# Kernel tuning notes

Measured on AMD Instinct MI355X. Metric: run time of the kernel, lower is better.

## Reference

```python
import jax, jax.numpy as jnp
import numpy as np

HIDDEN = 2048
VOCAB = 50257


def setup_inputs() -> dict:
    key = jax.random.key(0)
    ks = jax.random.split(key, 9)
    s = 0.02
    return {
        "token": jax.random.randint(ks[0], (1,), 0, VOCAB, dtype=jnp.int32),
        "hidden": jax.random.normal(ks[1], (1, 1, HIDDEN), dtype=jnp.float32),
        "emb": jax.random.normal(ks[2], (VOCAB, HIDDEN), dtype=jnp.float32) * s,
        "w_ih": jax.random.normal(ks[3], (3 * HIDDEN, HIDDEN), dtype=jnp.float32) * s,
        "w_hh": jax.random.normal(ks[4], (3 * HIDDEN, HIDDEN), dtype=jnp.float32) * s,
        "b_ih": jax.random.normal(ks[5], (3 * HIDDEN,), dtype=jnp.float32) * s,
        "b_hh": jax.random.normal(ks[6], (3 * HIDDEN,), dtype=jnp.float32) * s,
        "w_out": jax.random.normal(ks[7], (VOCAB, HIDDEN), dtype=jnp.float32) * s,
        "b_out": jax.random.normal(ks[8], (VOCAB,), dtype=jnp.float32) * s,
    }


def reference(token, hidden, emb, w_ih, w_hh, b_ih, b_hh, w_out, b_out):
    # embedding lookup + view(1,1,-1) + ReLU  -> x: [H]
    x = jax.nn.relu(emb[token].reshape(-1))
    h = hidden.reshape(-1)  # [H]
    # single GRU step (PyTorch gate order: r, z, n; separate input/hidden biases)
    gi = w_ih @ x + b_ih  # [3H]
    gh = w_hh @ h + b_hh  # [3H]
    i_r, i_z, i_n = jnp.split(gi, 3)
    h_r, h_z, h_n = jnp.split(gh, 3)
    r = jax.nn.sigmoid(i_r + h_r)
    z = jax.nn.sigmoid(i_z + h_z)
    n = jnp.tanh(i_n + r * h_n)
    h_new = (1.0 - z) * n + z * h  # [H]
    # output projection + log-softmax over vocab (dim=1 of [1, V])
    logits = w_out @ h_new + b_out  # [V]
    out = jax.nn.log_softmax(logits)[None, :]  # [1, V]
    return out, h_new.reshape(1, 1, -1)
```

## Files before the change

kernel.cpp:

```cpp
#include <hip/hip_runtime.h>
#include <math.h>

#define H 2048
#define G 6144
#define V 50257

#define WS_GI    0
#define WS_GH    G
#define WS_HNEW  12288
#define WS_MAX   14336
#define WS_SUM   14337
#define WS_LOGIT 14344

__device__ __forceinline__ float waveReduceSum(float v) {
  #pragma unroll
  for (int off = 32; off > 0; off >>= 1) v += __shfl_down(v, off, 64);
  return v;
}
__device__ __forceinline__ float waveReduceMax(float v) {
  #pragma unroll
  for (int off = 32; off > 0; off >>= 1) v = fmaxf(v, __shfl_down(v, off, 64));
  return v;
}

__device__ __forceinline__ unsigned orderedBits(float f) {
  unsigned u = __float_as_uint(f);
  return (u & 0x80000000u) ? ~u : (u | 0x80000000u);
}
__device__ __forceinline__ float orderedToFloat(unsigned m) {
  unsigned u = (m & 0x80000000u) ? (m & 0x7fffffffu) : ~m;
  return __uint_as_float(u);
}

__global__ __launch_bounds__(256) void gates_kernel(
    const int* __restrict__ token, const float* __restrict__ hidden,
    const float* __restrict__ emb, const float* __restrict__ w_ih,
    const float* __restrict__ w_hh, const float* __restrict__ b_ih,
    const float* __restrict__ b_hh, float* __restrict__ ws) {
  const int wave = threadIdx.x >> 6;
  const int lane = threadIdx.x & 63;
  const int row = blockIdx.x * 4 + wave;
  if (row >= G) return;
  const float4* x4 = (const float4*)(emb + (size_t)token[0] * H);
  const float4* h4 = (const float4*)hidden;
  const float4* wi = (const float4*)(w_ih + (size_t)row * H);
  const float4* wh = (const float4*)(w_hh + (size_t)row * H);
  float si = 0.f, sh = 0.f;
  #pragma unroll
  for (int k = 0; k < 8; ++k) {
    const int idx = k * 64 + lane;
    float4 a = wi[idx];
    float4 b = x4[idx];
    si += a.x * fmaxf(b.x, 0.f) + a.y * fmaxf(b.y, 0.f)
        + a.z * fmaxf(b.z, 0.f) + a.w * fmaxf(b.w, 0.f);
    float4 c = wh[idx];
    float4 d = h4[idx];
    sh += c.x * d.x + c.y * d.y + c.z * d.z + c.w * d.w;
  }
  si = waveReduceSum(si);
  sh = waveReduceSum(sh);
  if (lane == 0) {
    ws[WS_GI + row] = si + b_ih[row];
    ws[WS_GH + row] = sh + b_hh[row];
  }
}

__global__ __launch_bounds__(256) void hnew_kernel(
    const float* __restrict__ hidden, float* __restrict__ ws,
    float* __restrict__ out) {
  const int i = blockIdx.x * blockDim.x + threadIdx.x;
  if (i == 0) {
    ((unsigned*)ws)[WS_MAX] = 0u;
    ws[WS_SUM] = 0.f;
  }
  if (i < H) {
    const float r = 1.f / (1.f + expf(-(ws[WS_GI + i] + ws[WS_GH + i])));
    const float z = 1.f / (1.f + expf(-(ws[WS_GI + H + i] + ws[WS_GH + H + i])));
    const float n = tanhf(ws[WS_GI + 2 * H + i] + r * ws[WS_GH + 2 * H + i]);
    const float hn = (1.f - z) * n + z * hidden[i];
    ws[WS_HNEW + i] = hn;
    out[V + i] = hn;
  }
}

__global__ __launch_bounds__(256) void logits_kernel(
    const float* __restrict__ w_out, const float* __restrict__ b_out,
    float* __restrict__ ws) {
  const int wave = threadIdx.x >> 6;
  const int lane = threadIdx.x & 63;
  const int row = blockIdx.x * 4 + wave;
  if (row >= V) return;
  const float4* w4 = (const float4*)(w_out + (size_t)row * H);
  const float4* h4 = (const float4*)(ws + WS_HNEW);
  float s = 0.f;
  #pragma unroll
  for (int k = 0; k < 8; ++k) {
    const int idx = k * 64 + lane;
    float4 a = w4[idx];
    float4 b = h4[idx];
    s += a.x * b.x + a.y * b.y + a.z * b.z + a.w * b.w;
  }
  s = waveReduceSum(s);
  if (lane == 0) ws[WS_LOGIT + row] = s + b_out[row];
}

__global__ __launch_bounds__(256) void max_kernel(float* __restrict__ ws) {
  float m = -INFINITY;
  for (int i = blockIdx.x * blockDim.x + threadIdx.x; i < V;
       i += gridDim.x * blockDim.x)
    m = fmaxf(m, ws[WS_LOGIT + i]);
  m = waveReduceMax(m);
  __shared__ float sp[4];
  const int wave = threadIdx.x >> 6;
  const int lane = threadIdx.x & 63;
  if (lane == 0) sp[wave] = m;
  __syncthreads();
  if (threadIdx.x == 0) {
    const float bm = fmaxf(fmaxf(sp[0], sp[1]), fmaxf(sp[2], sp[3]));
    atomicMax((unsigned*)ws + WS_MAX, orderedBits(bm));
  }
}

__global__ __launch_bounds__(256) void sumexp_kernel(float* __restrict__ ws) {
  const float m = orderedToFloat(((const unsigned*)ws)[WS_MAX]);
  float s = 0.f;
  for (int i = blockIdx.x * blockDim.x + threadIdx.x; i < V;
       i += gridDim.x * blockDim.x)
    s += expf(ws[WS_LOGIT + i] - m);
  s = waveReduceSum(s);
  __shared__ float sp[4];
  const int wave = threadIdx.x >> 6;
  const int lane = threadIdx.x & 63;
  if (lane == 0) sp[wave] = s;
  __syncthreads();
  if (threadIdx.x == 0)
    atomicAdd(ws + WS_SUM, sp[0] + sp[1] + sp[2] + sp[3]);
}

__global__ __launch_bounds__(256) void writeout_kernel(
    const float* __restrict__ ws, float* __restrict__ out) {
  const int i = blockIdx.x * blockDim.x + threadIdx.x;
  if (i < V) {
    const float m = orderedToFloat(((const unsigned*)ws)[WS_MAX]);
    const float lse = m + logf(ws[WS_SUM]);
    out[i] = ws[WS_LOGIT + i] - lse;
  }
}

extern "C" void kernel_launch(void* const* d_in, const int* in_sizes, int n_in,
                              void* d_out, int out_size, void* d_ws, size_t ws_size,
                              hipStream_t stream) {
  const int*   token  = (const int*)  d_in[0];
  const float* hidden = (const float*)d_in[1];
  const float* emb    = (const float*)d_in[2];
  const float* w_ih   = (const float*)d_in[3];
  const float* w_hh   = (const float*)d_in[4];
  const float* b_ih   = (const float*)d_in[5];
  const float* b_hh   = (const float*)d_in[6];
  const float* w_out  = (const float*)d_in[7];
  const float* b_out  = (const float*)d_in[8];
  float* out = (float*)d_out;
  float* ws  = (float*)d_ws;

  gates_kernel<<<G / 4, 256, 0, stream>>>(token, hidden, emb, w_ih, w_hh,
                                          b_ih, b_hh, ws);
  hnew_kernel<<<(H + 255) / 256, 256, 0, stream>>>(hidden, ws, out);
  logits_kernel<<<(V + 3) / 4, 256, 0, stream>>>(w_out, b_out, ws);
  max_kernel<<<128, 256, 0, stream>>>(ws);
  sumexp_kernel<<<64, 256, 0, stream>>>(ws);
  writeout_kernel<<<(V + 255) / 256, 256, 0, stream>>>(ws, out);
}
```

Measured before the change: 753.0 us.

## Fuse GRU gate matvecs with hidden update and merge softmax reductions

The gate kernel now has each wave compute all six gate dot products for one hidden unit and apply the GRU nonlinearity directly, which removes the separate h_new kernel and its gate buffer round-trip. The max and sum-exp passes are merged into a single per-block kernel that writes partial max and partial sum, and writeout combines the 128 partials with an online-softmax rescale. This drops two launches and the atomics. In exchange, the gate kernel runs only 512 blocks, each streaming six rows, and every writeout block redundantly reduces all 128 partials.

```diff
diff --git a/kernel.cpp b/kernel.cpp
--- a/kernel.cpp
+++ b/kernel.cpp
@@ -4,13 +4,12 @@
 #define H 2048
 #define G 6144
 #define V 50257
+#define NPART 128
 
-#define WS_GI    0
-#define WS_GH    G
-#define WS_HNEW  12288
-#define WS_MAX   14336
-#define WS_SUM   14337
-#define WS_LOGIT 14344
+#define WS_HNEW  0
+#define WS_LOGIT 2048
+#define WS_PMAX  53248
+#define WS_PSUM  53376
 
 __device__ __forceinline__ float waveReduceSum(float v) {
   #pragma unroll
@@ -22,61 +21,54 @@
   for (int off = 32; off > 0; off >>= 1) v = fmaxf(v, __shfl_down(v, off, 64));
   return v;
 }
-
-__device__ __forceinline__ unsigned orderedBits(float f) {
-  unsigned u = __float_as_uint(f);
-  return (u & 0x80000000u) ? ~u : (u | 0x80000000u);
-}
-__device__ __forceinline__ float orderedToFloat(unsigned m) {
-  unsigned u = (m & 0x80000000u) ? (m & 0x7fffffffu) : ~m;
-  return __uint_as_float(u);
+__device__ __forceinline__ float sigmoidf(float x) {
+  return 1.f / (1.f + expf(-x));
 }
 
-__global__ __launch_bounds__(256) void gates_kernel(
+__global__ __launch_bounds__(256) void gru_kernel(
     const int* __restrict__ token, const float* __restrict__ hidden,
     const float* __restrict__ emb, const float* __restrict__ w_ih,
     const float* __restrict__ w_hh, const float* __restrict__ b_ih,
-    const float* __restrict__ b_hh, float* __restrict__ ws) {
+    const float* __restrict__ b_hh, float* __restrict__ ws,
+    float* __restrict__ out) {
   const int wave = threadIdx.x >> 6;
   const int lane = threadIdx.x & 63;
-  const int row = blockIdx.x * 4 + wave;
-  if (row >= G) return;
+  const int i = blockIdx.x * 4 + wave;
   const float4* x4 = (const float4*)(emb + (size_t)token[0] * H);
   const float4* h4 = (const float4*)hidden;
-  const float4* wi = (const float4*)(w_ih + (size_t)row * H);
-  const float4* wh = (const float4*)(w_hh + (size_t)row * H);
-  float si = 0.f, sh = 0.f;
+  const float4* wr_i = (const float4*)(w_ih + (size_t)i * H);
+  const float4* wz_i = (const float4*)(w_ih + (size_t)(H + i) * H);
+  const float4* wn_i = (const float4*)(w_ih + (size_t)(2 * H + i) * H);
+  const float4* wr_h = (const float4*)(w_hh + (size_t)i * H);
+  const float4* wz_h = (const float4*)(w_hh + (size_t)(H + i) * H);
+  const float4* wn_h = (const float4*)(w_hh + (size_t)(2 * H + i) * H);
+  float s_ir = 0.f, s_iz = 0.f, s_in = 0.f;
+  float s_hr = 0.f, s_hz = 0.f, s_hn = 0.f;
   #pragma unroll
   for (int k = 0; k < 8; ++k) {
     const int idx = k * 64 + lane;
-    float4 a = wi[idx];
-    float4 b = x4[idx];
-    si += a.x * fmaxf(b.x, 0.f) + a.y * fmaxf(b.y, 0.f)
-        + a.z * fmaxf(b.z, 0.f) + a.w * fmaxf(b.w, 0.f);
-    float4 c = wh[idx];
-    float4 d = h4[idx];
-    sh += c.x * d.x + c.y * d.y + c.z * d.z + c.w * d.w;
+    float4 xv = x4[idx];
+    xv.x = fmaxf(xv.x, 0.f); xv.y = fmaxf(xv.y, 0.f);
+    xv.z = fmaxf(xv.z, 0.f); xv.w = fmaxf(xv.w, 0.f);
+    float4 hv = h4[idx];
+    float4 a;
+    a = wr_i[idx]; s_ir += a.x*xv.x + a.y*xv.y + a.z*xv.z + a.w*xv.w;
+    a = wz_i[idx]; s_iz += a.x*xv.x + a.y*xv.y + a.z*xv.z + a.w*xv.w;
+    a = wn_i[idx]; s_in += a.x*xv.x + a.y*xv.y + a.z*xv.z + a.w*xv.w;
+    a = wr_h[idx]; s_hr += a.x*hv.x + a.y*hv.y + a.z*hv.z + a.w*hv.w;
+    a = wz_h[idx]; s_hz += a.x*hv.x + a.y*hv.y + a.z*hv.z + a.w*hv.w;
+    a = wn_h[idx]; s_hn += a.x*hv.x + a.y*hv.y + a.z*hv.z + a.w*hv.w;
   }
-  si = waveReduceSum(si);
-  sh = waveReduceSum(sh);
+  s_ir = waveReduceSum(s_ir);
+  s_iz = waveReduceSum(s_iz);
+  s_in = waveReduceSum(s_in);
+  s_hr = waveReduceSum(s_hr);
+  s_hz = waveReduceSum(s_hz);
+  s_hn = waveReduceSum(s_hn);
   if (lane == 0) {
-    ws[WS_GI + row] = si + b_ih[row];
-    ws[WS_GH + row] = sh + b_hh[row];
-  }
-}
-
-__global__ __launch_bounds__(256) void hnew_kernel(
-    const float* __restrict__ hidden, float* __restrict__ ws,
-    float* __restrict__ out) {
-  const int i = blockIdx.x * blockDim.x + threadIdx.x;
-  if (i == 0) {
-    ((unsigned*)ws)[WS_MAX] = 0u;
-    ws[WS_SUM] = 0.f;
-  }
-  if (i < H) {
-    const float r = 1.f / (1.f + expf(-(ws[WS_GI + i] + ws[WS_GH + i])));
-    const float z = 1.f / (1.f + expf(-(ws[WS_GI + H + i] + ws[WS_GH + H + i])));
-    const float n = tanhf(ws[WS_GI + 2 * H + i] + r * ws[WS_GH + 2 * H + i]);
+    const float r = sigmoidf(s_ir + b_ih[i] + s_hr + b_hh[i]);
+    const float z = sigmoidf(s_iz + b_ih[H + i] + s_hz + b_hh[H + i]);
+    const float n = tanhf(s_in + b_ih[2 * H + i] + r * (s_hn + b_hh[2 * H + i]));
     const float hn = (1.f - z) * n + z * hidden[i];
     ws[WS_HNEW + i] = hn;
     out[V + i] = hn;
@@ -104,47 +96,51 @@
   if (lane == 0) ws[WS_LOGIT + row] = s + b_out[row];
 }
 
-__global__ __launch_bounds__(256) void max_kernel(float* __restrict__ ws) {
+__global__ __launch_bounds__(256) void partial_kernel(float* __restrict__ ws) {
+  __shared__ float sred[4];
+  __shared__ float sbmax;
+  const int wave = threadIdx.x >> 6;
+  const int lane = threadIdx.x & 63;
   float m = -INFINITY;
-  for (int i = blockIdx.x * blockDim.x + threadIdx.x; i < V;
-       i += gridDim.x * blockDim.x)
+  for (int i = blockIdx.x * 256 + threadIdx.x; i < V; i += NPART * 256)
     m = fmaxf(m, ws[WS_LOGIT + i]);
   m = waveReduceMax(m);
-  __shared__ float sp[4];
-  const int wave = threadIdx.x >> 6;
-  const int lane = threadIdx.x & 63;
-  if (lane == 0) sp[wave] = m;
+  if (lane == 0) sred[wave] = m;
+  __syncthreads();
+  if (threadIdx.x == 0)
+    sbmax = fmaxf(fmaxf(sred[0], sred[1]), fmaxf(sred[2], sred[3]));
+  __syncthreads();
+  const float M = sbmax;
+  float s = 0.f;
+  for (int i = blockIdx.x * 256 + threadIdx.x; i < V; i += NPART * 256)
+    s += expf(ws[WS_LOGIT + i] - M);
+  s = waveReduceSum(s);
+  __syncthreads();
+  if (lane == 0) sred[wave] = s;
   __syncthreads();
   if (threadIdx.x == 0) {
-    const float bm = fmaxf(fmaxf(sp[0], sp[1]), fmaxf(sp[2], sp[3]));
-    atomicMax((unsigned*)ws + WS_MAX, orderedBits(bm));
+    ws[WS_PMAX + blockIdx.x] = M;
+    ws[WS_PSUM + blockIdx.x] = sred[0] + sred[1] + sred[2] + sred[3];
   }
-}
-
-__global__ __launch_bounds__(256) void sumexp_kernel(float* __restrict__ ws) {
-  const float m = orderedToFloat(((const unsigned*)ws)[WS_MAX]);
-  float s = 0.f;
-  for (int i = blockIdx.x * blockDim.x + threadIdx.x; i < V;
-       i += gridDim.x * blockDim.x)
-    s += expf(ws[WS_LOGIT + i] - m);
-  s = waveReduceSum(s);
-  __shared__ float sp[4];
-  const int wave = threadIdx.x >> 6;
-  const int lane = threadIdx.x & 63;
-  if (lane == 0) sp[wave] = s;
-  __syncthreads();
-  if (threadIdx.x == 0)
-    atomicAdd(ws + WS_SUM, sp[0] + sp[1] + sp[2] + sp[3]);
 }
 
 __global__ __launch_bounds__(256) void writeout_kernel(
     const float* __restrict__ ws, float* __restrict__ out) {
-  const int i = blockIdx.x * blockDim.x + threadIdx.x;
-  if (i < V) {
-    const float m = orderedToFloat(((const unsigned*)ws)[WS_MAX]);
-    const float lse = m + logf(ws[WS_SUM]);
-    out[i] = ws[WS_LOGIT + i] - lse;
+  __shared__ float pm[NPART], psv[NPART];
+  if (threadIdx.x < NPART) {
+    pm[threadIdx.x]  = ws[WS_PMAX + threadIdx.x];
+    psv[threadIdx.x] = ws[WS_PSUM + threadIdx.x];
   }
+  __syncthreads();
+  float M = -INFINITY;
+  #pragma unroll
+  for (int j = 0; j < NPART; ++j) M = fmaxf(M, pm[j]);
+  float S = 0.f;
+  #pragma unroll
+  for (int j = 0; j < NPART; ++j) S += psv[j] * expf(pm[j] - M);
+  const float lse = M + logf(S);
+  const int i = blockIdx.x * 256 + threadIdx.x;
+  if (i < V) out[i] = ws[WS_LOGIT + i] - lse;
 }
 
 extern "C" void kernel_launch(void* const* d_in, const int* in_sizes, int n_in,
@@ -162,11 +158,9 @@
   float* out = (float*)d_out;
   float* ws  = (float*)d_ws;
 
-  gates_kernel<<<G / 4, 256, 0, stream>>>(token, hidden, emb, w_ih, w_hh,
-                                          b_ih, b_hh, ws);
-  hnew_kernel<<<(H + 255) / 256, 256, 0, stream>>>(hidden, ws, out);
+  gru_kernel<<<H / 4, 256, 0, stream>>>(token, hidden, emb, w_ih, w_hh,
+                                        b_ih, b_hh, ws, out);
   logits_kernel<<<(V + 3) / 4, 256, 0, stream>>>(w_out, b_out, ws);
-  max_kernel<<<128, 256, 0, stream>>>(ws);
-  sumexp_kernel<<<64, 256, 0, stream>>>(ws);
+  partial_kernel<<<NPART, 256, 0, stream>>>(ws);
   writeout_kernel<<<(V + 255) / 256, 256, 0, stream>>>(ws, out);
 }
```

Measured after the change: 750.6 us. No clear change (-0.3%).
